# Kernel tuning notes

Measured on AMD Instinct MI355X. Metric: run time of the kernel, lower is better.

Reference implementation:

```python
import jax, jax.numpy as jnp
import numpy as np

B, T, I, D = 64, 128, 197, 768
FP16_MAX_NEG = -jnp.finfo(jnp.float16).max  # max_neg_value(fp16) = -65504


def setup_inputs() -> dict:
    key = jax.random.key(0)
    k1, k2, k3 = jax.random.split(key, 3)
    image_features = jax.random.normal(k1, (B, I, D), dtype=jnp.float32)
    text_features = jax.random.normal(k2, (B, T, D), dtype=jnp.float32)
    # realistic padding: each text has a random valid length in [T//2, T)
    lengths = jax.random.randint(k3, (B,), T // 2, T)
    padding_mask = (jnp.arange(T)[None, :] >= lengths[:, None]).astype(jnp.int32)
    logit_scale = jnp.ones((1,), dtype=jnp.float32)
    return {
        "image_features": image_features,
        "text_features": text_features,
        "padding_mask": padding_mask,
        "logit_scale": logit_scale,
    }


def _mask_eos(pm):
    # (pm==0).cumsum(1).argmax(1) = index of LAST zero (argmax returns first max)
    cum = jnp.cumsum((pm == 0).astype(jnp.int32), axis=1)
    last_zero = jnp.argmax(cum, axis=1)
    return pm.at[jnp.arange(pm.shape[0]), last_zero].set(1)


def _cmli(image_features, text_features, padding_mask, logit_scale):
    pm = _mask_eos(padding_mask)
    img = image_features.astype(jnp.float16)[:, 1:]   # [B, I-1, D]
    txt = text_features.astype(jnp.float16)[:, 1:]    # [B, T-1, D]
    pad = pm[:, 1:].astype(bool)                       # [B, T-1], True = padded

    scale = jnp.asarray(logit_scale, dtype=jnp.float16).reshape(())
    # sim[x, y, t, i] = <text token t of sample x, image patch i of sample y>
    sim = scale * jnp.einsum('xtd,yid->xyti', txt, img)  # [B, B, T-1, I-1] fp16

    # ---- text -> image: max over image patches, masked mean over text tokens
    t2i_tok = jnp.max(sim, axis=-1)                       # [x, y, t]
    mask_xt = pad[:, None, :]                             # [x, 1, t]
    numer = jnp.sum(jnp.where(mask_xt, jnp.float16(0.0), t2i_tok), axis=-1)
    denom = jnp.maximum(
        jnp.sum(~pad, axis=-1).astype(t2i_tok.dtype), jnp.float16(1e-6)
    )[:, None]                                            # [x, 1]
    t2i = numer / denom                                   # [B, B]

    # ---- image -> text: mask padded text tokens to -max, max over t, mean over i
    masked_sim = jnp.where(pad[:, None, :, None], jnp.float16(FP16_MAX_NEG), sim)
    i2t = jnp.mean(jnp.max(masked_sim, axis=2), axis=-1)  # [B, B]
    return i2t, t2i


def _cross_entropy_diag(logits):
    # labels = arange(B): diagonal positives; compute log_softmax in fp32
    logp = jax.nn.log_softmax(logits.astype(jnp.float32), axis=-1)
    n = logits.shape[0]
    return -jnp.mean(logp[jnp.arange(n), jnp.arange(n)])


def reference(image_features, text_features, padding_mask, logit_scale):
    i2t, t2i = _cmli(image_features, text_features, padding_mask, logit_scale)
    loss = (_cross_entropy_diag(i2t) + _cross_entropy_diag(t2i)) / 2
    return loss, i2t, t2i
```

## Files before the change

### kernel.cpp

```cpp
#include <hip/hip_runtime.h>
#include <stdint.h>

#define BB   64
#define TSEQ 128
#define ISEQ 197
#define DD   768
#define TM   127
#define IM   196
#define NK   24
#define A_KB (TM*64)
#define B_KB (IM*64)

typedef float    f32x4 __attribute__((ext_vector_type(4)));
typedef _Float16 h8    __attribute__((ext_vector_type(8)));
typedef _Float16 h4    __attribute__((ext_vector_type(4)));
typedef float    fvec4 __attribute__((ext_vector_type(4)));

__device__ __forceinline__ unsigned fkey(float f){
  unsigned u = __float_as_uint(f);
  return (u & 0x80000000u) ? ~u : (u | 0x80000000u);
}
__device__ __forceinline__ float fdekey(unsigned k){
  unsigned u = (k & 0x80000000u) ? (k & 0x7fffffffu) : ~k;
  return __uint_as_float(u);
}
__device__ __forceinline__ float waveSum(float v){
  #pragma unroll
  for (int s = 1; s < 64; s <<= 1) v += __shfl_xor(v, s, 64);
  return v;
}

__global__ void mask_kernel(const int* __restrict__ pmG, float* __restrict__ bias,
                            float* __restrict__ sel, int* __restrict__ cnt)
{
  int b = blockIdx.x; int l = threadIdx.x;
  const int* row = pmG + b*TSEQ;
  int p0 = row[l]; int p1 = row[l+64];
  unsigned long long m0 = __ballot(p0 == 0);
  unsigned long long m1 = __ballot(p1 == 0);
  int lz = 0;
  if (m1)      lz = 64 + (63 - __clzll(m1));
  else if (m0) lz = 63 - __clzll(m0);
  int t1 = l + 1;
  int q1 = row[t1];
  bool v1 = (q1 == 0) && (t1 != lz);
  int t2 = l + 65;
  bool v2 = false;
  if (t2 < TSEQ){ int q2 = row[t2]; v2 = (q2 == 0) && (t2 != lz); }
  bias[b*128 + l]      = v1 ? 0.f : -3.0e38f;
  sel [b*128 + l]      = v1 ? 1.f : 0.f;
  bias[b*128 + 64 + l] = v2 ? 0.f : -3.0e38f;
  sel [b*128 + 64 + l] = v2 ? 1.f : 0.f;
  unsigned long long vm1 = __ballot(v1);
  unsigned long long vm2 = __ballot(v2);
  if (l == 0) cnt[b] = __popcll(vm1) + __popcll(vm2);
}

__global__ void cvt_txt_kernel(const float* __restrict__ src, _Float16* __restrict__ dst){
  int t = blockIdx.x;
  int b = blockIdx.y;
  int i = threadIdx.x;
  const fvec4* s = (const fvec4*)(src + ((size_t)b*TSEQ + t + 1)*DD) + i;
  fvec4 v = *s;
  h4 h; h.x=(_Float16)v.x; h.y=(_Float16)v.y; h.z=(_Float16)v.z; h.w=(_Float16)v.w;
  int ks = i >> 3; int o = (i & 7)*4;
  _Float16* d = dst + (size_t)b*(NK*TM*32) + (size_t)ks*(TM*32) + t*32 + o;
  *(h4*)d = h;
}
__global__ void cvt_img_kernel(const float* __restrict__ src, _Float16* __restrict__ dst){
  int t = blockIdx.x;
  int b = blockIdx.y;
  int i = threadIdx.x;
  const fvec4* s = (const fvec4*)(src + ((size_t)b*ISEQ + t + 1)*DD) + i;
  fvec4 v = *s;
  h4 h; h.x=(_Float16)v.x; h.y=(_Float16)v.y; h.z=(_Float16)v.z; h.w=(_Float16)v.w;
  int ks = i >> 3; int o = (i & 7)*4;
  _Float16* d = dst + (size_t)b*(NK*IM*32) + (size_t)ks*(IM*32) + t*32 + o;
  *(h4*)d = h;
}

__global__ __launch_bounds__(256, 2)
void cmli_pair_kernel(const _Float16* __restrict__ txtH,
                      const _Float16* __restrict__ imgH,
                      const float* __restrict__ biasG,
                      const float* __restrict__ selG,
                      const int* __restrict__ cntG,
                      const float* __restrict__ scaleP,
                      float* __restrict__ out)
{
  __shared__ __align__(16) char smem[45056 + 512 + 896 + 64];
  unsigned* rowKeys = (unsigned*)(smem + 45056);
  unsigned* colKeys = (unsigned*)(smem + 45056 + 512);
  float*    parts   = (float*)(smem + 45056 + 512 + 896);

  const int tid  = threadIdx.x;
  const int lane = tid & 63;
  const int w    = tid >> 6;
  const int wm   = w & 1;
  const int wn   = w >> 1;
  const int bx   = blockIdx.x >> 6;
  const int by   = blockIdx.x & 63;

  const char* tA = (const char*)txtH + (size_t)bx * (NK*A_KB);
  const char* tB = (const char*)imgH + (size_t)by * (NK*B_KB);

  const int pg   = (lane>>4) ^ ((lane>>1)&3);
  const int aOff = (wm*64  + (lane&15))*64 + pg*16;
  const int bOff = (wn*112 + (lane&15))*64 + pg*16;

  int sA[2], dA[2], sB[4], dB[4];
  #pragma unroll
  for (int i=0;i<2;i++){
    int c = tid + 256*i; int r = c>>2; int p = c&3; int g = p ^ ((r>>1)&3);
    sA[i] = min(r,126)*64 + g*16; dA[i] = c*16;
  }
  #pragma unroll
  for (int i=0;i<4;i++){
    int c = tid + 256*i; int r = c>>2; int p = c&3; int g = p ^ ((r>>1)&3);
    sB[i] = min(r,195)*64 + g*16; dB[i] = c*16;
  }
  const bool hasB3 = (tid < 128);

  f32x4 acc[4][7];
  #pragma unroll
  for (int m=0;m<4;m++)
    #pragma unroll
    for (int n=0;n<7;n++)
      acc[m][n] = (f32x4){0.f,0.f,0.f,0.f};

  if (tid < 128) rowKeys[tid] = 0u;
  if (tid < 224) colKeys[tid] = 0u;

  {
    uint4 va0 = *(const uint4*)(tA + sA[0]);
    uint4 va1 = *(const uint4*)(tA + sA[1]);
    uint4 vb0 = *(const uint4*)(tB + sB[0]);
    uint4 vb1 = *(const uint4*)(tB + sB[1]);
    uint4 vb2 = *(const uint4*)(tB + sB[2]);
    uint4 vb3;
    if (hasB3) vb3 = *(const uint4*)(tB + sB[3]);
    char* A0 = smem; char* B0 = smem + 8192;
    *(uint4*)(A0 + dA[0]) = va0;
    *(uint4*)(A0 + dA[1]) = va1;
    *(uint4*)(B0 + dB[0]) = vb0;
    *(uint4*)(B0 + dB[1]) = vb1;
    *(uint4*)(B0 + dB[2]) = vb2;
    if (hasB3) *(uint4*)(B0 + dB[3]) = vb3;
  }
  __syncthreads();

  for (int ks=0; ks<NK; ks++){
    const int cur = ks & 1;
    uint4 va0,va1,vb0,vb1,vb2,vb3;
    if (ks+1 < NK){
      const char* at = tA + (size_t)(ks+1)*A_KB;
      const char* bt = tB + (size_t)(ks+1)*B_KB;
      va0 = *(const uint4*)(at + sA[0]);
      va1 = *(const uint4*)(at + sA[1]);
      vb0 = *(const uint4*)(bt + sB[0]);
      vb1 = *(const uint4*)(bt + sB[1]);
      vb2 = *(const uint4*)(bt + sB[2]);
      if (hasB3) vb3 = *(const uint4*)(bt + sB[3]);
    }
    const char* Ab = smem + (cur ? 22528 : 0);
    const char* Bb = smem + (cur ? 30720 : 8192);
    h8 af[4]; h8 bf[7];
    #pragma unroll
    for (int m=0;m<4;m++) af[m] = *(const h8*)(Ab + aOff + m*1024);
    #pragma unroll
    for (int n=0;n<7;n++) bf[n] = *(const h8*)(Bb + bOff + n*1024);
    #pragma unroll
    for (int m=0;m<4;m++)
      #pragma unroll
      for (int n=0;n<7;n++)
        acc[m][n] = __builtin_amdgcn_mfma_f32_16x16x32_f16(af[m], bf[n], acc[m][n], 0,0,0);
    if (ks+1 < NK){
      char* An = smem + (cur ? 0 : 22528);
      char* Bn = smem + (cur ? 8192 : 30720);
      *(uint4*)(An + dA[0]) = va0;
      *(uint4*)(An + dA[1]) = va1;
      *(uint4*)(Bn + dB[0]) = vb0;
      *(uint4*)(Bn + dB[1]) = vb1;
      *(uint4*)(Bn + dB[2]) = vb2;
      if (hasB3) *(uint4*)(Bn + dB[3]) = vb3;
    }
    __syncthreads();
  }

  const float scale = scaleP[0];
  #pragma unroll
  for (int m=0;m<4;m++)
    #pragma unroll
    for (int n=0;n<7;n++)
      acc[m][n] *= scale;

  #pragma unroll
  for (int m=0;m<4;m++){
    f32x4 r = acc[m][0];
    #pragma unroll
    for (int n=1;n<7;n++){
      r.x = fmaxf(r.x, acc[m][n].x); r.y = fmaxf(r.y, acc[m][n].y);
      r.z = fmaxf(r.z, acc[m][n].z); r.w = fmaxf(r.w, acc[m][n].w);
    }
    #pragma unroll
    for (int s=1;s<16;s<<=1){
      r.x = fmaxf(r.x, __shfl_xor(r.x, s, 64));
      r.y = fmaxf(r.y, __shfl_xor(r.y, s, 64));
      r.z = fmaxf(r.z, __shfl_xor(r.z, s, 64));
      r.w = fmaxf(r.w, __shfl_xor(r.w, s, 64));
    }
    if ((lane & 15) == 0){
      int row = wm*64 + m*16 + (lane>>4)*4;
      atomicMax(&rowKeys[row+0], fkey(r.x));
      atomicMax(&rowKeys[row+1], fkey(r.y));
      atomicMax(&rowKeys[row+2], fkey(r.z));
      atomicMax(&rowKeys[row+3], fkey(r.w));
    }
  }

  fvec4 bv[4];
  #pragma unroll
  for (int m=0;m<4;m++)
    bv[m] = *(const fvec4*)(biasG + bx*128 + wm*64 + m*16 + (lane>>4)*4);
  #pragma unroll
  for (int n=0;n<7;n++){
    float c = -3.0e38f;
    #pragma unroll
    for (int m=0;m<4;m++){
      c = fmaxf(c, acc[m][n].x + bv[m].x);
      c = fmaxf(c, acc[m][n].y + bv[m].y);
      c = fmaxf(c, acc[m][n].z + bv[m].z);
      c = fmaxf(c, acc[m][n].w + bv[m].w);
    }
    c = fmaxf(c, __shfl_xor(c, 16, 64));
    c = fmaxf(c, __shfl_xor(c, 32, 64));
    if (lane < 16){
      int col = wn*112 + n*16 + lane;
      atomicMax(&colKeys[col], fkey(c));
    }
  }
  __syncthreads();

  float v = 0.f;
  if (tid < 128){
    float s = selG[bx*128 + tid];
    v = (s > 0.5f) ? fdekey(rowKeys[tid]) : 0.f;
  }
  float u = (tid < IM) ? fdekey(colKeys[tid]) : 0.f;
  v = waveSum(v); u = waveSum(u);
  if (lane == 0){ parts[w] = v; parts[4+w] = u; }
  __syncthreads();
  if (tid == 0){
    float numer = parts[0]+parts[1]+parts[2]+parts[3];
    float csum  = parts[4]+parts[5]+parts[6]+parts[7];
    float denom = fmaxf((float)cntG[bx], 1e-6f);
    out[1 + 4096 + blockIdx.x] = numer / denom;
    out[1 + blockIdx.x]        = csum * (1.f/196.f);
  }
}

__global__ void loss_kernel(float* __restrict__ out){
  __shared__ float p[2];
  int w = threadIdx.x >> 6, lane = threadIdx.x & 63;
  const float* M = out + 1 + w*4096;
  const float* r = M + lane*64;
  float mx = -3.0e38f;
  for (int j=0;j<64;j++) mx = fmaxf(mx, r[j]);
  float se = 0.f;
  for (int j=0;j<64;j++) se += __expf(r[j]-mx);
  float nll = (mx + __logf(se)) - r[lane];
  float s = waveSum(nll);
  if (lane == 0) p[w] = s;
  __syncthreads();
  if (threadIdx.x == 0) out[0] = (p[0] + p[1]) * (0.5f/64.f);
}

extern "C" void kernel_launch(void* const* d_in, const int* in_sizes, int n_in,
                              void* d_out, int out_size, void* d_ws, size_t ws_size,
                              hipStream_t stream)
{
  const float* imgF   = (const float*)d_in[0];
  const float* txtF   = (const float*)d_in[1];
  const int*   pm     = (const int*)d_in[2];
  const float* scaleP = (const float*)d_in[3];
  float* out = (float*)d_out;

  char* ws = (char*)d_ws;
  _Float16* txtH = (_Float16*)ws;
  _Float16* imgH = (_Float16*)(ws + 12484608);
  float* bias = (float*)(ws + 31752192);
  float* sel  = (float*)(ws + 31784960);
  int*   cnt  = (int*)(ws + 31817728);

  hipLaunchKernelGGL(mask_kernel,    dim3(BB),      dim3(64),  0, stream, pm, bias, sel, cnt);
  hipLaunchKernelGGL(cvt_txt_kernel, dim3(TM, BB),  dim3(192), 0, stream, txtF, txtH);
  hipLaunchKernelGGL(cvt_img_kernel, dim3(IM, BB),  dim3(192), 0, stream, imgF, imgH);
  hipLaunchKernelGGL(cmli_pair_kernel, dim3(BB*BB), dim3(256), 0, stream,
                     txtH, imgH, bias, sel, cnt, scaleP, out);
  hipLaunchKernelGGL(loss_kernel,    dim3(1),       dim3(128), 0, stream, out);
}
```

Measured before the change: 213.0 us.

## Use direct global-to-LDS loads with deeper B buffering and skip padded row tiles

```diff
diff --git a/kernel.cpp b/kernel.cpp
--- a/kernel.cpp
+++ b/kernel.cpp
@@ -11,6 +11,12 @@
 #define A_KB (TM*64)
 #define B_KB (IM*64)
 
+#define LDS_B0   16384
+#define LDS_RK   59392
+#define LDS_CK   59904
+#define LDS_PT   60800
+#define LDS_TOT  60864
+
 typedef float    f32x4 __attribute__((ext_vector_type(4)));
 typedef _Float16 h8    __attribute__((ext_vector_type(8)));
 typedef _Float16 h4    __attribute__((ext_vector_type(4)));
@@ -28,6 +34,12 @@
   #pragma unroll
   for (int s = 1; s < 64; s <<= 1) v += __shfl_xor(v, s, 64);
   return v;
+}
+
+__device__ __forceinline__ void gload_lds16(const void* g, void* l){
+  __builtin_amdgcn_global_load_lds(
+      (const __attribute__((address_space(1))) void*)g,
+      (__attribute__((address_space(3))) void*)l, 16, 0, 0);
 }
 
 __global__ void mask_kernel(const int* __restrict__ pmG, float* __restrict__ bias,
@@ -88,10 +100,10 @@
                       const float* __restrict__ scaleP,
                       float* __restrict__ out)
 {
-  __shared__ __align__(16) char smem[45056 + 512 + 896 + 64];
-  unsigned* rowKeys = (unsigned*)(smem + 45056);
-  unsigned* colKeys = (unsigned*)(smem + 45056 + 512);
-  float*    parts   = (float*)(smem + 45056 + 512 + 896);
+  __shared__ __align__(16) char smem[LDS_TOT];
+  unsigned* rowKeys = (unsigned*)(smem + LDS_RK);
+  unsigned* colKeys = (unsigned*)(smem + LDS_CK);
+  float*    parts   = (float*)(smem + LDS_PT);
 
   const int tid  = threadIdx.x;
   const int lane = tid & 63;
@@ -103,134 +115,150 @@
 
   const char* tA = (const char*)txtH + (size_t)bx * (NK*A_KB);
   const char* tB = (const char*)imgH + (size_t)by * (NK*B_KB);
-
-  const int pg   = (lane>>4) ^ ((lane>>1)&3);
-  const int aOff = (wm*64  + (lane&15))*64 + pg*16;
-  const int bOff = (wn*112 + (lane&15))*64 + pg*16;
-
-  int sA[2], dA[2], sB[4], dB[4];
+  const int mtc = (cntG[bx] + 15) >> 4;
+
+  int aSrc[2], aLds[2];
   #pragma unroll
   for (int i=0;i<2;i++){
-    int c = tid + 256*i; int r = c>>2; int p = c&3; int g = p ^ ((r>>1)&3);
-    sA[i] = min(r,126)*64 + g*16; dA[i] = c*16;
-  }
+    int c = w + 4*i; int p = c*64 + lane; int r = p>>2; int pg = p&3;
+    int g = pg ^ ((r>>1)&3);
+    aSrc[i] = min(r,126)*64 + g*16; aLds[i] = c*1024;
+  }
+  const int kB = (w < 2) ? 4 : 3;
+  int bSrc[4], bLds[4];
   #pragma unroll
   for (int i=0;i<4;i++){
-    int c = tid + 256*i; int r = c>>2; int p = c&3; int g = p ^ ((r>>1)&3);
-    sB[i] = min(r,195)*64 + g*16; dB[i] = c*16;
-  }
-  const bool hasB3 = (tid < 128);
+    int c = w + 4*i; if (c > 13) c = 13;
+    int p = c*64 + lane; int r = p>>2; int pg = p&3;
+    int g = pg ^ ((r>>1)&3);
+    bSrc[i] = min(r,195)*64 + g*16; bLds[i] = c*1024;
+  }
+
+  const int pgf  = (lane>>4) ^ ((lane>>1)&3);
+  const int aOff = (lane&15)*64 + pgf*16;
+  const int bOff = (wn*112 + (lane&15))*64 + pgf*16;
 
   f32x4 acc[4][7];
   #pragma unroll
-  for (int m=0;m<4;m++)
+  for (int j=0;j<4;j++)
     #pragma unroll
     for (int n=0;n<7;n++)
-      acc[m][n] = (f32x4){0.f,0.f,0.f,0.f};
+      acc[j][n] = (f32x4){0.f,0.f,0.f,0.f};
 
   if (tid < 128) rowKeys[tid] = 0u;
   if (tid < 224) colKeys[tid] = 0u;
 
   {
-    uint4 va0 = *(const uint4*)(tA + sA[0]);
-    uint4 va1 = *(const uint4*)(tA + sA[1]);
-    uint4 vb0 = *(const uint4*)(tB + sB[0]);
-    uint4 vb1 = *(const uint4*)(tB + sB[1]);
-    uint4 vb2 = *(const uint4*)(tB + sB[2]);
-    uint4 vb3;
-    if (hasB3) vb3 = *(const uint4*)(tB + sB[3]);
-    char* A0 = smem; char* B0 = smem + 8192;
-    *(uint4*)(A0 + dA[0]) = va0;
-    *(uint4*)(A0 + dA[1]) = va1;
-    *(uint4*)(B0 + dB[0]) = vb0;
-    *(uint4*)(B0 + dB[1]) = vb1;
-    *(uint4*)(B0 + dB[2]) = vb2;
-    if (hasB3) *(uint4*)(B0 + dB[3]) = vb3;
-  }
-  __syncthreads();
-
-  for (int ks=0; ks<NK; ks++){
-    const int cur = ks & 1;
-    uint4 va0,va1,vb0,vb1,vb2,vb3;
-    if (ks+1 < NK){
-      const char* at = tA + (size_t)(ks+1)*A_KB;
-      const char* bt = tB + (size_t)(ks+1)*B_KB;
-      va0 = *(const uint4*)(at + sA[0]);
-      va1 = *(const uint4*)(at + sA[1]);
-      vb0 = *(const uint4*)(bt + sB[0]);
-      vb1 = *(const uint4*)(bt + sB[1]);
-      vb2 = *(const uint4*)(bt + sB[2]);
-      if (hasB3) vb3 = *(const uint4*)(bt + sB[3]);
-    }
-    const char* Ab = smem + (cur ? 22528 : 0);
-    const char* Bb = smem + (cur ? 30720 : 8192);
+    #pragma unroll
+    for (int i=0;i<4;i++) if (i < kB) gload_lds16(tB + bSrc[i], smem + LDS_B0 + bLds[i]);
+    #pragma unroll
+    for (int i=0;i<2;i++) gload_lds16(tA + aSrc[i], smem + aLds[i]);
+    const char* bt1 = tB + B_KB;
+    #pragma unroll
+    for (int i=0;i<4;i++) if (i < kB) gload_lds16(bt1 + bSrc[i], smem + LDS_B0 + 14336 + bLds[i]);
+    if (w < 2) asm volatile("s_waitcnt vmcnt(4)" ::: "memory");
+    else       asm volatile("s_waitcnt vmcnt(3)" ::: "memory");
+    __builtin_amdgcn_s_barrier();
+    asm volatile("" ::: "memory");
+  }
+
+  int rbA = 0, rbB = 0;
+  for (int t=0; t<NK; t++){
+    {
+      int ka  = (t+1 < NK) ? t+1 : NK-1;
+      int kb2 = (t+2 < NK) ? t+2 : NK-1;
+      const char* at = tA + (size_t)ka  * A_KB;
+      const char* bt = tB + (size_t)kb2 * B_KB;
+      int aBase = (rbA ^ 1) * 8192;
+      int sb3 = rbB + 2; if (sb3 >= 3) sb3 -= 3;
+      int bBase = LDS_B0 + sb3 * 14336;
+      #pragma unroll
+      for (int i=0;i<2;i++) gload_lds16(at + aSrc[i], smem + aBase + aLds[i]);
+      #pragma unroll
+      for (int i=0;i<4;i++) if (i < kB) gload_lds16(bt + bSrc[i], smem + bBase + bLds[i]);
+    }
+    const char* Ab = smem + rbA*8192;
+    const char* Bb = smem + LDS_B0 + rbB*14336;
     h8 af[4]; h8 bf[7];
     #pragma unroll
-    for (int m=0;m<4;m++) af[m] = *(const h8*)(Ab + aOff + m*1024);
-    #pragma unroll
     for (int n=0;n<7;n++) bf[n] = *(const h8*)(Bb + bOff + n*1024);
     #pragma unroll
-    for (int m=0;m<4;m++)
-      #pragma unroll
-      for (int n=0;n<7;n++)
-        acc[m][n] = __builtin_amdgcn_mfma_f32_16x16x32_f16(af[m], bf[n], acc[m][n], 0,0,0);
-    if (ks+1 < NK){
-      char* An = smem + (cur ? 0 : 22528);
-      char* Bn = smem + (cur ? 8192 : 30720);
-      *(uint4*)(An + dA[0]) = va0;
-      *(uint4*)(An + dA[1]) = va1;
-      *(uint4*)(Bn + dB[0]) = vb0;
-      *(uint4*)(Bn + dB[1]) = vb1;
-      *(uint4*)(Bn + dB[2]) = vb2;
-      if (hasB3) *(uint4*)(Bn + dB[3]) = vb3;
-    }
-    __syncthreads();
+    for (int j=0;j<4;j++){
+      int g = wm + 2*j;
+      if (g < mtc) af[j] = *(const h8*)(Ab + aOff + g*1024);
+    }
+    #pragma unroll
+    for (int j=0;j<4;j++){
+      int g = wm + 2*j;
+      if (g < mtc){
+        #pragma unroll
+        for (int n=0;n<7;n++)
+          acc[j][n] = __builtin_amdgcn_mfma_f32_16x16x32_f16(af[j], bf[n], acc[j][n], 0,0,0);
+      }
+    }
+    if (w < 2) asm volatile("s_waitcnt vmcnt(4)" ::: "memory");
+    else       asm volatile("s_waitcnt vmcnt(3)" ::: "memory");
+    __builtin_amdgcn_s_barrier();
+    asm volatile("" ::: "memory");
+    rbA ^= 1; rbB = (rbB == 2) ? 0 : rbB + 1;
   }
 
   const float scale = scaleP[0];
   #pragma unroll
-  for (int m=0;m<4;m++)
-    #pragma unroll
-    for (int n=0;n<7;n++)
-      acc[m][n] *= scale;
-
-  #pragma unroll
-  for (int m=0;m<4;m++){
-    f32x4 r = acc[m][0];
-    #pragma unroll
-    for (int n=1;n<7;n++){
-      r.x = fmaxf(r.x, acc[m][n].x); r.y = fmaxf(r.y, acc[m][n].y);
-      r.z = fmaxf(r.z, acc[m][n].z); r.w = fmaxf(r.w, acc[m][n].w);
-    }
-    #pragma unroll
-    for (int s=1;s<16;s<<=1){
-      r.x = fmaxf(r.x, __shfl_xor(r.x, s, 64));
-      r.y = fmaxf(r.y, __shfl_xor(r.y, s, 64));
-      r.z = fmaxf(r.z, __shfl_xor(r.z, s, 64));
-      r.w = fmaxf(r.w, __shfl_xor(r.w, s, 64));
-    }
-    if ((lane & 15) == 0){
-      int row = wm*64 + m*16 + (lane>>4)*4;
-      atomicMax(&rowKeys[row+0], fkey(r.x));
-      atomicMax(&rowKeys[row+1], fkey(r.y));
-      atomicMax(&rowKeys[row+2], fkey(r.z));
-      atomicMax(&rowKeys[row+3], fkey(r.w));
+  for (int j=0;j<4;j++){
+    int g = wm + 2*j;
+    if (g < mtc){
+      #pragma unroll
+      for (int n=0;n<7;n++) acc[j][n] *= scale;
+    }
+  }
+
+  #pragma unroll
+  for (int j=0;j<4;j++){
+    int g = wm + 2*j;
+    if (g < mtc){
+      f32x4 r = acc[j][0];
+      #pragma unroll
+      for (int n=1;n<7;n++){
+        r.x = fmaxf(r.x, acc[j][n].x); r.y = fmaxf(r.y, acc[j][n].y);
+        r.z = fmaxf(r.z, acc[j][n].z); r.w = fmaxf(r.w, acc[j][n].w);
+      }
+      #pragma unroll
+      for (int s=1;s<16;s<<=1){
+        r.x = fmaxf(r.x, __shfl_xor(r.x, s, 64));
+        r.y = fmaxf(r.y, __shfl_xor(r.y, s, 64));
+        r.z = fmaxf(r.z, __shfl_xor(r.z, s, 64));
+        r.w = fmaxf(r.w, __shfl_xor(r.w, s, 64));
+      }
+      if ((lane & 15) == 0){
+        int row = g*16 + (lane>>4)*4;
+        atomicMax(&rowKeys[row+0], fkey(r.x));
+        atomicMax(&rowKeys[row+1], fkey(r.y));
+        atomicMax(&rowKeys[row+2], fkey(r.z));
+        atomicMax(&rowKeys[row+3], fkey(r.w));
+      }
     }
   }
 
   fvec4 bv[4];
   #pragma unroll
-  for (int m=0;m<4;m++)
-    bv[m] = *(const fvec4*)(biasG + bx*128 + wm*64 + m*16 + (lane>>4)*4);
+  for (int j=0;j<4;j++){
+    int g = wm + 2*j;
+    if (g < mtc)
+      bv[j] = *(const fvec4*)(biasG + bx*128 + g*16 + (lane>>4)*4);
+  }
   #pragma unroll
   for (int n=0;n<7;n++){
     float c = -3.0e38f;
     #pragma unroll
-    for (int m=0;m<4;m++){
-      c = fmaxf(c, acc[m][n].x + bv[m].x);
-      c = fmaxf(c, acc[m][n].y + bv[m].y);
-      c = fmaxf(c, acc[m][n].z + bv[m].z);
-      c = fmaxf(c, acc[m][n].w + bv[m].w);
+    for (int j=0;j<4;j++){
+      int g = wm + 2*j;
+      if (g < mtc){
+        c = fmaxf(c, acc[j][n].x + bv[j].x);
+        c = fmaxf(c, acc[j][n].y + bv[j].y);
+        c = fmaxf(c, acc[j][n].z + bv[j].z);
+        c = fmaxf(c, acc[j][n].w + bv[j].w);
+      }
     }
     c = fmaxf(c, __shfl_xor(c, 16, 64));
     c = fmaxf(c, __shfl_xor(c, 32, 64));
```

After: 201.2 us. 5.5% less time.
